# Kernel tuning notes

Hardware: AMD Instinct MI355X
Metric: run time of the kernel (lower is better)

## Reference

```python
import jax, jax.numpy as jnp
import numpy as np

N = 25600            # 64 graphs x 400 ROIs
F_IN = 400
H = 128
E = 512000           # 8000 edges per graph
B = 64
G = 8
OUT = 2
NPG = 400            # nodes per graph
EPG = E // B         # edges per graph
BN_EPS = 1e-5


def _xavier(k, shape):
    lim = float(np.sqrt(6.0 / (shape[0] + shape[1])))
    return jax.random.uniform(k, shape, jnp.float32, -lim, lim)


def setup_inputs() -> dict:
    key = jax.random.key(0)
    ks = jax.random.split(key, 16)
    inp = {}
    inp["x"] = jax.random.normal(ks[0], (N, F_IN), jnp.float32)
    # within-graph random edges: local index + graph offset
    src_l = jax.random.randint(ks[1], (E,), 0, NPG, jnp.int32)
    dst_l = jax.random.randint(ks[2], (E,), 0, NPG, jnp.int32)
    off = (jnp.arange(E, dtype=jnp.int32) // EPG) * NPG
    inp["edge_index"] = jnp.stack([src_l + off, dst_l + off])
    inp["batch"] = (jnp.arange(N, dtype=jnp.int32) // NPG)
    inp["group_ids"] = jax.random.randint(ks[3], (N,), 0, G, jnp.int32)
    inp["ge"] = _xavier(ks[4], (G, 2))
    inp["he"] = _xavier(ks[5], (2, 2))
    dims = [(F_IN + 4, H), (H, H), (H, H)]
    for i, (di, do) in enumerate(dims):
        k1, k2 = jax.random.split(ks[6 + i])
        inp[f"w{i}a"] = _xavier(k1, (di, do))
        inp[f"b{i}a"] = jnp.zeros((do,), jnp.float32)
        inp[f"g{i}"] = jnp.ones((do,), jnp.float32)
        inp[f"be{i}"] = jnp.zeros((do,), jnp.float32)
        inp[f"w{i}b"] = _xavier(k2, (do, do))
        inp[f"b{i}b"] = jnp.zeros((do,), jnp.float32)
    inp["wfa"] = _xavier(ks[10], (H, H))
    inp["bfa"] = jnp.zeros((H,), jnp.float32)
    inp["wfb"] = _xavier(ks[11], (H, OUT))
    inp["bfb"] = jnp.zeros((OUT,), jnp.float32)
    return inp


def _bn(h, gamma, beta):
    # BatchNorm1d in training mode: stats over node dimension
    mu = jnp.mean(h, axis=0, keepdims=True)
    var = jnp.var(h, axis=0, keepdims=True)
    return gamma * (h - mu) * jax.lax.rsqrt(var + BN_EPS) + beta


def reference(x, edge_index, batch, group_ids, ge, he,
              w0a, b0a, g0, be0, w0b, b0b,
              w1a, b1a, g1, be1, w1b, b1b,
              w2a, b2a, g2, be2, w2b, b2b,
              wfa, bfa, wfb, bfb):
    n = x.shape[0]
    hemi = jnp.arange(n) % 2                      # [1::2] = 1
    h = jnp.concatenate([x, ge[group_ids], he[hemi]], axis=-1)  # [N, F_IN+4]
    src, dst = edge_index[0], edge_index[1]
    layers = [(w0a, b0a, g0, be0, w0b, b0b),
              (w1a, b1a, g1, be1, w1b, b1b),
              (w2a, b2a, g2, be2, w2b, b2b)]
    for wa, ba, g, be, wb, bb in layers:
        # GINConv (eps=0): x_i + sum_{(j,i)} x_j, then 2-layer MLP w/ batchnorm
        agg = jax.ops.segment_sum(h[src], dst, num_segments=N)
        z = h + agg
        z = jax.nn.relu(_bn(z @ wa + ba, g, be))  # dropout = identity (eval)
        h = jax.nn.relu(z @ wb + bb)              # outer ReLU from forward()
    pooled = jax.ops.segment_sum(h, batch, num_segments=B)  # global_add_pool
    return jax.nn.relu(pooled @ wfa + bfa) @ wfb + bfb
```

## Files before the change

### kernel.cpp

```cpp
#include <hip/hip_runtime.h>

#define N_NODES 25600
#define F_IN 400
#define NE 512000
#define NB 64
#define NPG 400
#define EPG 8000
#define BN_EPS 1e-5f

#define S_ROWS 448
#define S_COLS 448
#define S_COLS2 (S_COLS / 2)
#define AGG_TILES 7
#define SB_RPB 112
#define K0PAD 448

typedef __attribute__((ext_vector_type(8))) short short8;
typedef __attribute__((ext_vector_type(4))) short short4_t;
typedef __attribute__((ext_vector_type(4))) float floatx4;

__device__ __forceinline__ unsigned short f2bf(float f) {
    unsigned int u = __float_as_uint(f);
    u += 0x7FFF + ((u >> 16) & 1);
    return (unsigned short)(u >> 16);
}
__device__ __forceinline__ float bf2f(unsigned short s) {
    return __uint_as_float((unsigned int)s << 16);
}
__device__ __forceinline__ short u8bf(unsigned v) {
    return (short)(__float_as_uint((float)v) >> 16);
}


__global__ __launch_bounds__(256) void prep(const int* __restrict__ src,
                                            const int* __restrict__ dst,
                                            unsigned char* __restrict__ Sb,
                                            const float* __restrict__ wa0, const float* __restrict__ wa1,
                                            const float* __restrict__ wa2, const float* __restrict__ wb0,
                                            const float* __restrict__ wb1, const float* __restrict__ wb2,
                                            unsigned short* __restrict__ t0, unsigned short* __restrict__ t1,
                                            unsigned short* __restrict__ t2, unsigned short* __restrict__ t3,
                                            unsigned short* __restrict__ t4, unsigned short* __restrict__ t5,
                                            float* __restrict__ pstat) {
    __shared__ int cnt32[SB_RPB * NPG / 4];
    int tid = threadIdx.x;
    if (blockIdx.x < 256) {
        int b = blockIdx.x;
        int g = b >> 2, part = b & 3;
        int r0 = part * SB_RPB;
        for (int i = tid; i < SB_RPB * NPG / 4; i += 256) cnt32[i] = 0;
        __syncthreads();
        int ebase = g * EPG, nbase = g * NPG;
        for (int e = tid; e < EPG; e += 256) {
            int d = dst[ebase + e] - nbase;
            int dr = d - r0;
            if ((unsigned)dr < (unsigned)SB_RPB) {
                int s = src[ebase + e] - nbase;
                int idx = dr * NPG + s;
                atomicAdd(&cnt32[idx >> 2], (int)(1u << ((idx & 3) * 8)));
            }
        }
        __syncthreads();
        const unsigned char* cb = (const unsigned char*)cnt32;
        for (int i = tid; i < SB_RPB * (S_COLS / 8); i += 256) {
            int rr = i / (S_COLS / 8), c8 = (i % (S_COLS / 8)) * 8;
            int R = r0 + rr;
            unsigned pk = 0;
#pragma unroll
            for (int j = 0; j < 8; ++j) {
                int c = c8 + j;
                unsigned v = 0;
                if (R < NPG && c < NPG) v = (unsigned)cb[rr * NPG + c] + (c == R ? 1u : 0u);
                pk |= (v & 15u) << (4 * j);
            }
            *(unsigned*)&Sb[((size_t)g * S_ROWS + R) * S_COLS2 + (c8 >> 1)] = pk;
        }
        return;
    }
    int idx = (blockIdx.x - 256) * 256 + tid;
    if (idx < 3 * 2048 + 8192) pstat[idx] = 0.f;
    if (idx < 128 * K0PAD) {
        int n = idx / K0PAD, k = idx - n * K0PAD;
        t0[idx] = (k < 400) ? f2bf(wa0[(size_t)k * 128 + n]) : (unsigned short)0;
        return;
    }
    idx -= 128 * K0PAD;
    if (idx >= 5 * 128 * 128) return;
    int seg = idx >> 14;
    int r = idx & 16383;
    int n = r >> 7, k = r & 127;
    const float* srcs[5] = {wb0, wa1, wb1, wa2, wb2};
    unsigned short* dsts[5] = {t3, t1, t4, t2, t5};
    dsts[seg][r] = f2bf(srcs[seg][(size_t)k * 128 + n]);
}


__global__ __launch_bounds__(256) void gemm_embed64(const float* __restrict__ A,
                                                    const unsigned short* __restrict__ Wt,
                                                    const float* __restrict__ Wfull,
                                                    const int* __restrict__ gid,
                                                    const float* __restrict__ ge,
                                                    const float* __restrict__ he,
                                                    unsigned short* __restrict__ CtT) {
    __shared__ __align__(16) unsigned short As[64][72];
    __shared__ __align__(16) unsigned short Bs[128][72];
    __shared__ float Wex[4][128];
    int tid = threadIdx.x;
    int m0 = blockIdx.x * 64;
    int wave = tid >> 6, lane = tid & 63;
    int wcol = wave * 32;
    int fm = lane & 15, quad = lane >> 4;

    for (int i = tid; i < 512; i += 256)
        Wex[i >> 7][i & 127] = Wfull[(size_t)(400 + (i >> 7)) * 128 + (i & 127)];

    floatx4 acc[4][2];
#pragma unroll
    for (int rt = 0; rt < 4; ++rt)
#pragma unroll
        for (int ct = 0; ct < 2; ++ct) acc[rt][ct] = (floatx4){0.f, 0.f, 0.f, 0.f};

    const int rA = tid >> 2, kcA = (tid & 3) * 16;
    const int nB = tid >> 1, kcB = (tid & 1) * 32;
    float4 aP0, aP1, aP2, aP3;
    short8 bP0, bP1, bP2, bP3;

    auto loadK = [&](int ks) {
        int k0 = ks * 64;
        int kg = k0 + kcA;
        const float* ar = A + (size_t)(m0 + rA) * F_IN;
        if (kg + 15 < 400) {
            aP0 = *(const float4*)(ar + kg);
            aP1 = *(const float4*)(ar + kg + 4);
            aP2 = *(const float4*)(ar + kg + 8);
            aP3 = *(const float4*)(ar + kg + 12);
        } else {
            float v[16];
#pragma unroll
            for (int j = 0; j < 16; ++j) v[j] = (kg + j < 400) ? ar[kg + j] : 0.f;
            aP0 = (float4){v[0], v[1], v[2], v[3]};
            aP1 = (float4){v[4], v[5], v[6], v[7]};
            aP2 = (float4){v[8], v[9], v[10], v[11]};
            aP3 = (float4){v[12], v[13], v[14], v[15]};
        }
        const unsigned short* wr = Wt + (size_t)nB * K0PAD + k0 + kcB;
        bP0 = *(const short8*)wr;
        bP1 = *(const short8*)(wr + 8);
        bP2 = *(const short8*)(wr + 16);
        bP3 = *(const short8*)(wr + 24);
    };

    loadK(0);
    for (int ks = 0; ks < 7; ++ks) {
        {
            short8 s0, s1;
            s0[0] = (short)f2bf(aP0.x); s0[1] = (short)f2bf(aP0.y);
            s0[2] = (short)f2bf(aP0.z); s0[3] = (short)f2bf(aP0.w);
            s0[4] = (short)f2bf(aP1.x); s0[5] = (short)f2bf(aP1.y);
            s0[6] = (short)f2bf(aP1.z); s0[7] = (short)f2bf(aP1.w);
            s1[0] = (short)f2bf(aP2.x); s1[1] = (short)f2bf(aP2.y);
            s1[2] = (short)f2bf(aP2.z); s1[3] = (short)f2bf(aP2.w);
            s1[4] = (short)f2bf(aP3.x); s1[5] = (short)f2bf(aP3.y);
            s1[6] = (short)f2bf(aP3.z); s1[7] = (short)f2bf(aP3.w);
            *(short8*)&As[rA][kcA] = s0;
            *(short8*)&As[rA][kcA + 8] = s1;
            *(short8*)&Bs[nB][kcB] = bP0;
            *(short8*)&Bs[nB][kcB + 8] = bP1;
            *(short8*)&Bs[nB][kcB + 16] = bP2;
            *(short8*)&Bs[nB][kcB + 24] = bP3;
        }
        __syncthreads();
        if (ks + 1 < 7) loadK(ks + 1);
#pragma unroll
        for (int k0l = 0; k0l < 64; k0l += 32) {
            short8 af[4], bf[2];
#pragma unroll
            for (int rt = 0; rt < 4; ++rt)
                af[rt] = *(const short8*)&As[rt * 16 + fm][k0l + quad * 8];
#pragma unroll
            for (int ct = 0; ct < 2; ++ct)
                bf[ct] = *(const short8*)&Bs[wcol + ct * 16 + fm][k0l + quad * 8];
#pragma unroll
            for (int rt = 0; rt < 4; ++rt)
#pragma unroll
                for (int ct = 0; ct < 2; ++ct)
                    acc[rt][ct] = __builtin_amdgcn_mfma_f32_16x16x32_bf16(
                        af[rt], bf[ct], acc[rt][ct], 0, 0, 0);
        }
        __syncthreads();
    }

#pragma unroll
    for (int rt = 0; rt < 4; ++rt) {
#pragma unroll
        for (int ct = 0; ct < 2; ++ct) {
            int col = wcol + ct * 16 + fm;
            int row0 = m0 + rt * 16 + quad * 4;
            ushort4 o;
#pragma unroll
            for (int r = 0; r < 4; ++r) {
                int row = row0 + r;
                int gv = gid[row];
                float v = acc[rt][ct][r]
                        + ge[gv * 2] * Wex[0][col] + ge[gv * 2 + 1] * Wex[1][col]
                        + he[(row & 1) * 2] * Wex[2][col] + he[(row & 1) * 2 + 1] * Wex[3][col];
                ((unsigned short*)&o)[r] = f2bf(v);
            }
            *(ushort4*)&CtT[(size_t)col * N_NODES + row0] = o;
        }
    }
}


__global__ __launch_bounds__(256) void agg_mfma(const unsigned char* __restrict__ Sb,
                                                const unsigned short* __restrict__ tT,
                                                const float* __restrict__ bias,
                                                unsigned short* __restrict__ z,
                                                float* __restrict__ psumG,
                                                float* __restrict__ psqG) {
    __shared__ __align__(16) unsigned short As[64][72];
    __shared__ __align__(16) unsigned short Bs[128][72];
    __shared__ float sw[4][2][16], qw[4][2][16];
    int tid = threadIdx.x;
    int b = blockIdx.x;
    int g = b & 63;
    int tile = b >> 6;
    int m0l = tile * 64;
    int node0 = g * NPG;
    int wave = tid >> 6, lane = tid & 63;
    int wcol = wave * 32;
    int fm = lane & 15, quad = lane >> 4;

    floatx4 acc[4][2];
#pragma unroll
    for (int rt = 0; rt < 4; ++rt)
#pragma unroll
        for (int ct = 0; ct < 2; ++ct) acc[rt][ct] = (floatx4){0.f, 0.f, 0.f, 0.f};

    const int rA = tid >> 2, kcA = (tid & 3) * 16;
    const int nB = tid >> 1, kcB = (tid & 1) * 32;
    unsigned long long aP;
    short8 bP0, bP1, bP2, bP3;

    auto loadK = [&](int ks) {
        int k0 = ks * 64;
        aP = *(const unsigned long long*)(Sb + ((size_t)g * S_ROWS + m0l + rA) * S_COLS2 + ((k0 + kcA) >> 1));
        const unsigned short* p = tT + (size_t)nB * N_NODES + node0 + k0 + kcB;
        bP0 = *(const short8*)p;
        bP1 = *(const short8*)(p + 8);
        bP2 = *(const short8*)(p + 16);
        bP3 = *(const short8*)(p + 24);
    };

    loadK(0);
    for (int ks = 0; ks < S_COLS / 64; ++ks) {
        {
            short8 s0, s1;
#pragma unroll
            for (int j = 0; j < 8; ++j) s0[j] = u8bf((unsigned)(aP >> (4 * j)) & 15u);
#pragma unroll
            for (int j = 0; j < 8; ++j) s1[j] = u8bf((unsigned)(aP >> (32 + 4 * j)) & 15u);
            *(short8*)&As[rA][kcA] = s0;
            *(short8*)&As[rA][kcA + 8] = s1;
            *(short8*)&Bs[nB][kcB] = bP0;
            *(short8*)&Bs[nB][kcB + 8] = bP1;
            *(short8*)&Bs[nB][kcB + 16] = bP2;
            *(short8*)&Bs[nB][kcB + 24] = bP3;
        }
        __syncthreads();
        if (ks + 1 < S_COLS / 64) loadK(ks + 1);
#pragma unroll
        for (int k0l = 0; k0l < 64; k0l += 32) {
            short8 af[4], bf[2];
#pragma unroll
            for (int rt = 0; rt < 4; ++rt)
                af[rt] = *(const short8*)&As[rt * 16 + fm][k0l + quad * 8];
#pragma unroll
            for (int ct = 0; ct < 2; ++ct)
                bf[ct] = *(const short8*)&Bs[wcol + ct * 16 + fm][k0l + quad * 8];
#pragma unroll
            for (int rt = 0; rt < 4; ++rt)
#pragma unroll
                for (int ct = 0; ct < 2; ++ct)
                    acc[rt][ct] = __builtin_amdgcn_mfma_f32_16x16x32_bf16(
                        af[rt], bf[ct], acc[rt][ct], 0, 0, 0);
        }
        __syncthreads();
    }

    {
        float scol[2] = {0.f, 0.f}, qcol[2] = {0.f, 0.f};
#pragma unroll
        for (int rt = 0; rt < 4; ++rt) {
#pragma unroll
            for (int ct = 0; ct < 2; ++ct) {
                int col = wcol + ct * 16 + fm;
                float bv = bias[col];
                int rbase = m0l + rt * 16 + quad * 4;
#pragma unroll
                for (int r = 0; r < 4; ++r) {
                    int rloc = rbase + r;
                    if (rloc < NPG) {
                        float v = acc[rt][ct][r] + bv;
                        z[(size_t)(node0 + rloc) * 128 + col] = f2bf(v);
                        scol[ct] += v;
                        qcol[ct] += v * v;
                    }
                }
            }
        }
#pragma unroll
        for (int ct = 0; ct < 2; ++ct) {
            scol[ct] += __shfl_xor(scol[ct], 16);
            scol[ct] += __shfl_xor(scol[ct], 32);
            qcol[ct] += __shfl_xor(qcol[ct], 16);
            qcol[ct] += __shfl_xor(qcol[ct], 32);
        }
        if (lane < 16) {
#pragma unroll
            for (int ct = 0; ct < 2; ++ct) { sw[wave][ct][lane] = scol[ct]; qw[wave][ct][lane] = qcol[ct]; }
        }
    }
    __syncthreads();
    if (tid < 128) {
        int c = tid;
        int wv = c >> 5, ct = (c >> 4) & 1, f = c & 15;
        int bucket = b & 7;
        atomicAdd(&psumG[bucket * 128 + c], sw[wv][ct][f]);
        atomicAdd(&psqG[bucket * 128 + c], qw[wv][ct][f]);
    }
}


#define MODE_FUSED 0
#define MODE_FINAL 1

template <int MODE>
__global__ __launch_bounds__(256) void gemm_post64(const unsigned short* __restrict__ z,
                                                   const float* __restrict__ psumG,
                                                   const float* __restrict__ psqG,
                                                   const float* __restrict__ gamma,
                                                   const float* __restrict__ beta,
                                                   const unsigned short* __restrict__ wtb,
                                                   const float* __restrict__ bb,
                                                   const unsigned short* __restrict__ wta_next,
                                                   unsigned short* __restrict__ CtT,
                                                   float* __restrict__ pooled) {
    __shared__ __align__(16) unsigned short Bs[128][72];
    __shared__ __align__(16) unsigned short hs[64][136];
    __shared__ float coefs[256];
    int tid = threadIdx.x;
    int m0 = blockIdx.x * 64;
    int wave = tid >> 6, lane = tid & 63;
    int wcol = wave * 32;
    int fm = lane & 15, quad = lane >> 4;

    if (tid < 128) {
        float S = 0.f, Q = 0.f;
#pragma unroll
        for (int b = 0; b < 8; ++b) { S += psumG[b * 128 + tid]; Q += psqG[b * 128 + tid]; }
        float invn = 1.0f / (float)N_NODES;
        float mu = S * invn;
        float var = Q * invn - mu * mu;
        float a = gamma[tid] * rsqrtf(var + BN_EPS);
        coefs[tid] = a;
        coefs[128 + tid] = beta[tid] - a * mu;
    }
    __syncthreads();

    floatx4 acc[4][2];
#pragma unroll
    for (int rt = 0; rt < 4; ++rt)
#pragma unroll
        for (int ct = 0; ct < 2; ++ct) acc[rt][ct] = (floatx4){0.f, 0.f, 0.f, 0.f};

    const int rA = tid >> 2, kcA = (tid & 3) * 16;
    const int nB = tid >> 1, kcB = (tid & 1) * 32;
    short8 aPa, aPb;
    short8 bP0, bP1, bP2, bP3;

    auto loadK1 = [&](int ks) {
        int k0 = ks * 64;
        const unsigned short* zr = &z[(size_t)(m0 + rA) * 128 + k0 + kcA];
        aPa = *(const short8*)zr;
        aPb = *(const short8*)(zr + 8);
        const unsigned short* wr = wtb + (size_t)nB * 128 + k0 + kcB;
        bP0 = *(const short8*)wr;
        bP1 = *(const short8*)(wr + 8);
        bP2 = *(const short8*)(wr + 16);
        bP3 = *(const short8*)(wr + 24);
    };

    loadK1(0);
    for (int ks = 0; ks < 2; ++ks) {
        {
            int kg = ks * 64 + kcA;
            short8 s0, s1;
#pragma unroll
            for (int j = 0; j < 8; ++j) {
                float v = fmaxf(coefs[kg + j] * bf2f((unsigned short)aPa[j]) + coefs[128 + kg + j], 0.f);
                s0[j] = (short)f2bf(v);
            }
#pragma unroll
            for (int j = 0; j < 8; ++j) {
                float v = fmaxf(coefs[kg + 8 + j] * bf2f((unsigned short)aPb[j]) + coefs[128 + kg + 8 + j], 0.f);
                s1[j] = (short)f2bf(v);
            }
            *(short8*)&hs[rA][kcA] = s0;
            *(short8*)&hs[rA][kcA + 8] = s1;
            *(short8*)&Bs[nB][kcB] = bP0;
            *(short8*)&Bs[nB][kcB + 8] = bP1;
            *(short8*)&Bs[nB][kcB + 16] = bP2;
            *(short8*)&Bs[nB][kcB + 24] = bP3;
        }
        __syncthreads();
        if (ks + 1 < 2) loadK1(ks + 1);
#pragma unroll
        for (int k0l = 0; k0l < 64; k0l += 32) {
            short8 af[4], bf[2];
#pragma unroll
            for (int rt = 0; rt < 4; ++rt)
                af[rt] = *(const short8*)&hs[rt * 16 + fm][k0l + quad * 8];
#pragma unroll
            for (int ct = 0; ct < 2; ++ct)
                bf[ct] = *(const short8*)&Bs[wcol + ct * 16 + fm][k0l + quad * 8];
#pragma unroll
            for (int rt = 0; rt < 4; ++rt)
#pragma unroll
                for (int ct = 0; ct < 2; ++ct)
                    acc[rt][ct] = __builtin_amdgcn_mfma_f32_16x16x32_bf16(
                        af[rt], bf[ct], acc[rt][ct], 0, 0, 0);
        }
        __syncthreads();
    }

    if (MODE == MODE_FINAL) {
        float rsum[4][2];
#pragma unroll
        for (int rt = 0; rt < 4; ++rt)
#pragma unroll
            for (int ct = 0; ct < 2; ++ct) {
                int col = wcol + ct * 16 + fm;
                float bv = bb[col];
                float s = 0.f;
#pragma unroll
                for (int r = 0; r < 4; ++r) s += fmaxf(acc[rt][ct][r] + bv, 0.f);
                rsum[rt][ct] = s;
            }
        bool uniform = (m0 / NPG) == ((m0 + 63) / NPG);
        if (uniform) {
            int gph = m0 / NPG;
#pragma unroll
            for (int ct = 0; ct < 2; ++ct) {
                float cs = rsum[0][ct] + rsum[1][ct] + rsum[2][ct] + rsum[3][ct];
                cs += __shfl_xor(cs, 16);
                cs += __shfl_xor(cs, 32);
                if (lane < 16) atomicAdd(&pooled[gph * 128 + wcol + ct * 16 + fm], cs);
            }
        } else {
#pragma unroll
            for (int rt = 0; rt < 4; ++rt)
#pragma unroll
                for (int ct = 0; ct < 2; ++ct) {
                    int gph = (m0 + rt * 16 + quad * 4) / NPG;
                    atomicAdd(&pooled[gph * 128 + wcol + ct * 16 + fm], rsum[rt][ct]);
                }
        }
        return;
    }

#pragma unroll
    for (int rt = 0; rt < 4; ++rt)
#pragma unroll
        for (int ct = 0; ct < 2; ++ct) {
            int col = wcol + ct * 16 + fm;
            float bv = bb[col];
            int rbase = rt * 16 + quad * 4;
#pragma unroll
            for (int r = 0; r < 4; ++r)
                hs[rbase + r][col] = f2bf(fmaxf(acc[rt][ct][r] + bv, 0.f));
        }
    __syncthreads();

#pragma unroll
    for (int rt = 0; rt < 4; ++rt)
#pragma unroll
        for (int ct = 0; ct < 2; ++ct) acc[rt][ct] = (floatx4){0.f, 0.f, 0.f, 0.f};

    const int kcB2 = (tid & 1) * 16;
    for (int ks = 0; ks < 4; ++ks) {
        int k0 = ks * 32;
        {
            const unsigned short* wr = wta_next + (size_t)nB * 128 + k0 + kcB2;
            *(short8*)&Bs[nB][kcB2] = *(const short8*)wr;
            *(short8*)&Bs[nB][kcB2 + 8] = *(const short8*)(wr + 8);
        }
        __syncthreads();
        {
            short8 af[4], bf[2];
#pragma unroll
            for (int rt = 0; rt < 4; ++rt)
                af[rt] = *(const short8*)&hs[rt * 16 + fm][k0 + quad * 8];
#pragma unroll
            for (int ct = 0; ct < 2; ++ct)
                bf[ct] = *(const short8*)&Bs[wcol + ct * 16 + fm][quad * 8];
#pragma unroll
            for (int rt = 0; rt < 4; ++rt)
#pragma unroll
                for (int ct = 0; ct < 2; ++ct)
                    acc[rt][ct] = __builtin_amdgcn_mfma_f32_16x16x32_bf16(
                        af[rt], bf[ct], acc[rt][ct], 0, 0, 0);
        }
        __syncthreads();
    }

#pragma unroll
    for (int rt = 0; rt < 4; ++rt)
#pragma unroll
        for (int ct = 0; ct < 2; ++ct) {
            int col = wcol + ct * 16 + fm;
            int row0 = m0 + rt * 16 + quad * 4;
            ushort4 o;
#pragma unroll
            for (int r = 0; r < 4; ++r) ((unsigned short*)&o)[r] = f2bf(acc[rt][ct][r]);
            *(ushort4*)&CtT[(size_t)col * N_NODES + row0] = o;
        }
}


__global__ __launch_bounds__(128) void head(const float* __restrict__ pooled,
                                            const float* __restrict__ wfa,
                                            const float* __restrict__ bfa,
                                            const float* __restrict__ wfb,
                                            const float* __restrict__ bfb,
                                            float* __restrict__ out) {
    int g = blockIdx.x;
    int f = threadIdx.x;
    __shared__ float pl[128];
    pl[f] = pooled[g * 128 + f];
    __syncthreads();
    float a = bfa[f];
    for (int k = 0; k < 128; ++k) a += pl[k] * wfa[k * 128 + f];
    float p2 = fmaxf(a, 0.f);
    __shared__ float o0[128], o1[128];
    o0[f] = p2 * wfb[f * 2 + 0];
    o1[f] = p2 * wfb[f * 2 + 1];
    __syncthreads();
    if (f == 0) {
        float a0 = bfb[0], a1 = bfb[1];
#pragma unroll
        for (int k = 0; k < 128; ++k) { a0 += o0[k]; a1 += o1[k]; }
        out[g * 2 + 0] = a0;
        out[g * 2 + 1] = a1;
    }
}


extern "C" void kernel_launch(void* const* d_in, const int* in_sizes, int n_in,
                              void* d_out, int out_size, void* d_ws, size_t ws_size,
                              hipStream_t stream) {
    const float* x   = (const float*)d_in[0];
    const int* ei    = (const int*)d_in[1];
    const int* gid   = (const int*)d_in[3];
    const float* ge  = (const float*)d_in[4];
    const float* he  = (const float*)d_in[5];
    const float* wa[3] = {(const float*)d_in[6],  (const float*)d_in[12], (const float*)d_in[18]};
    const float* ba[3] = {(const float*)d_in[7],  (const float*)d_in[13], (const float*)d_in[19]};
    const float* gg[3] = {(const float*)d_in[8],  (const float*)d_in[14], (const float*)d_in[20]};
    const float* bb_[3]= {(const float*)d_in[9],  (const float*)d_in[15], (const float*)d_in[21]};
    const float* wb[3] = {(const float*)d_in[10], (const float*)d_in[16], (const float*)d_in[22]};
    const float* bbias[3] = {(const float*)d_in[11], (const float*)d_in[17], (const float*)d_in[23]};
    const float* wfa = (const float*)d_in[24];
    const float* bfa = (const float*)d_in[25];
    const float* wfb = (const float*)d_in[26];
    const float* bfb = (const float*)d_in[27];
    float* out = (float*)d_out;

    char* ws = (char*)d_ws;
    size_t o = 0;
    auto alloc = [&](size_t bytes) { char* p = ws + o; o += (bytes + 255) & ~(size_t)255; return p; };
    unsigned short* tT = (unsigned short*)alloc((size_t)128 * N_NODES * 2 + 1024);
    unsigned short* z  = (unsigned short*)alloc((size_t)N_NODES * 128 * 2);
    unsigned char* Sb  = (unsigned char*)alloc((size_t)NB * S_ROWS * S_COLS2);
    float* pstat = (float*)alloc((3 * 2048 + 8192) * 4);
    unsigned short* wt0  = (unsigned short*)alloc(128 * K0PAD * 2);
    unsigned short* wta1 = (unsigned short*)alloc(128 * 128 * 2);
    unsigned short* wta2 = (unsigned short*)alloc(128 * 128 * 2);
    unsigned short* wtb0 = (unsigned short*)alloc(128 * 128 * 2);
    unsigned short* wtb1 = (unsigned short*)alloc(128 * 128 * 2);
    unsigned short* wtb2 = (unsigned short*)alloc(128 * 128 * 2);
    (void)ws_size; (void)in_sizes; (void)n_in; (void)out_size;

    const int* esrc_in = ei;
    const int* edst_in = ei + NE;

    prep<<<256 + 544, 256, 0, stream>>>(esrc_in, edst_in, Sb,
                                        wa[0], wa[1], wa[2], wb[0], wb[1], wb[2],
                                        wt0, wta1, wta2, wtb0, wtb1, wtb2, pstat);

    float* ps0 = pstat;            float* pq0 = pstat + 1024;
    float* ps1 = pstat + 2048;     float* pq1 = pstat + 3072;
    float* ps2 = pstat + 4096;     float* pq2 = pstat + 5120;
    float* pooled = pstat + 6144;

    gemm_embed64<<<400, 256, 0, stream>>>(x, wt0, wa[0], gid, ge, he, tT);
    agg_mfma<<<NB * AGG_TILES, 256, 0, stream>>>(Sb, tT, ba[0], z, ps0, pq0);
    gemm_post64<MODE_FUSED><<<400, 256, 0, stream>>>(z, ps0, pq0, gg[0], bb_[0],
                                                     wtb0, bbias[0], wta1, tT, nullptr);
    agg_mfma<<<NB * AGG_TILES, 256, 0, stream>>>(Sb, tT, ba[1], z, ps1, pq1);
    gemm_post64<MODE_FUSED><<<400, 256, 0, stream>>>(z, ps1, pq1, gg[1], bb_[1],
                                                     wtb1, bbias[1], wta2, tT, nullptr);
    agg_mfma<<<NB * AGG_TILES, 256, 0, stream>>>(Sb, tT, ba[2], z, ps2, pq2);
    gemm_post64<MODE_FINAL><<<400, 256, 0, stream>>>(z, ps2, pq2, gg[2], bb_[2],
                                                     wtb2, bbias[2], nullptr, nullptr, pooled);

    head<<<NB, 128, 0, stream>>>(pooled, wfa, bfa, wfb, bfb, out);
}
```

Before: 254.1 us.

## Fuse all GIN stages into one persistent kernel with grid-wide barriers

Replaces the nine separate launches (prep, embed, three agg/post pairs, head) with one persistent kernel of 448 blocks that runs each phase in turn, separated by a software grid barrier built on atomics. Shared memory is carved by hand per phase, and the weight-transpose prep loops over several passes so fewer blocks cover it. This removes launch overhead and inter-kernel gaps. In exchange it relies on all 448 blocks being co-resident (launch_bounds 256,2) and adds barrier spin cost plus a memset per call.

```diff
diff --git a/kernel.cpp b/kernel.cpp
--- a/kernel.cpp
+++ b/kernel.cpp
@@ -11,13 +11,26 @@
 #define S_ROWS 448
 #define S_COLS 448
 #define S_COLS2 (S_COLS / 2)
-#define AGG_TILES 7
 #define SB_RPB 112
 #define K0PAD 448
 
+#define NBLK 448
+
+#define TT_OFF    0u
+#define Z_OFF     6555648u
+#define SB_OFF    13109248u
+#define PSTAT_OFF 19531776u
+#define WT0_OFF   19589120u
+#define WTA1_OFF  19703808u
+#define WTA2_OFF  19736576u
+#define WTB0_OFF  19769344u
+#define WTB1_OFF  19802112u
+#define WTB2_OFF  19834880u
+#define BAR_OFF   19867648u
+
 typedef __attribute__((ext_vector_type(8))) short short8;
-typedef __attribute__((ext_vector_type(4))) short short4_t;
 typedef __attribute__((ext_vector_type(4))) float floatx4;
+typedef unsigned short us;
 
 __device__ __forceinline__ unsigned short f2bf(float f) {
     unsigned int u = __float_as_uint(f);
@@ -31,22 +44,33 @@
     return (short)(__float_as_uint((float)v) >> 16);
 }
 
-
-__global__ __launch_bounds__(256) void prep(const int* __restrict__ src,
-                                            const int* __restrict__ dst,
-                                            unsigned char* __restrict__ Sb,
-                                            const float* __restrict__ wa0, const float* __restrict__ wa1,
-                                            const float* __restrict__ wa2, const float* __restrict__ wb0,
-                                            const float* __restrict__ wb1, const float* __restrict__ wb2,
-                                            unsigned short* __restrict__ t0, unsigned short* __restrict__ t1,
-                                            unsigned short* __restrict__ t2, unsigned short* __restrict__ t3,
-                                            unsigned short* __restrict__ t4, unsigned short* __restrict__ t5,
-                                            float* __restrict__ pstat) {
-    __shared__ int cnt32[SB_RPB * NPG / 4];
-    int tid = threadIdx.x;
-    if (blockIdx.x < 256) {
-        int b = blockIdx.x;
-        int g = b >> 2, part = b & 3;
+__device__ __forceinline__ void gsync(unsigned* bar) {
+    __syncthreads();
+    if (threadIdx.x == 0) {
+        unsigned gen = __hip_atomic_load(bar + 16, __ATOMIC_ACQUIRE, __HIP_MEMORY_SCOPE_AGENT);
+        __threadfence();
+        if (__hip_atomic_fetch_add(bar, 1u, __ATOMIC_ACQ_REL, __HIP_MEMORY_SCOPE_AGENT) == NBLK - 1u) {
+            __hip_atomic_store(bar, 0u, __ATOMIC_RELAXED, __HIP_MEMORY_SCOPE_AGENT);
+            __hip_atomic_fetch_add(bar + 16, 1u, __ATOMIC_RELEASE, __HIP_MEMORY_SCOPE_AGENT);
+        } else {
+            while (__hip_atomic_load(bar + 16, __ATOMIC_RELAXED, __HIP_MEMORY_SCOPE_AGENT) == gen)
+                __builtin_amdgcn_s_sleep(8);
+        }
+        __threadfence();
+    }
+    __syncthreads();
+}
+
+
+__device__ __forceinline__ void phase_prep(unsigned char* smem, int bid, int tid,
+        const int* __restrict__ src, const int* __restrict__ dst, unsigned char* Sb,
+        const float* __restrict__ wa0, const float* __restrict__ wa1, const float* __restrict__ wa2,
+        const float* __restrict__ wb0, const float* __restrict__ wb1, const float* __restrict__ wb2,
+        us* wt0, us* wta1, us* wta2, us* wtb0, us* wtb1, us* wtb2,
+        float* pstat, us* tT) {
+    if (bid < 256) {
+        int* cnt32 = (int*)smem;
+        int g = bid >> 2, part = bid & 3;
         int r0 = part * SB_RPB;
         for (int i = tid; i < SB_RPB * NPG / 4; i += 256) cnt32[i] = 0;
         __syncthreads();
@@ -75,38 +99,38 @@
             }
             *(unsigned*)&Sb[((size_t)g * S_ROWS + R) * S_COLS2 + (c8 >> 1)] = pk;
         }
-        return;
-    }
-    int idx = (blockIdx.x - 256) * 256 + tid;
-    if (idx < 3 * 2048 + 8192) pstat[idx] = 0.f;
-    if (idx < 128 * K0PAD) {
-        int n = idx / K0PAD, k = idx - n * K0PAD;
-        t0[idx] = (k < 400) ? f2bf(wa0[(size_t)k * 128 + n]) : (unsigned short)0;
-        return;
-    }
-    idx -= 128 * K0PAD;
-    if (idx >= 5 * 128 * 128) return;
-    int seg = idx >> 14;
-    int r = idx & 16383;
-    int n = r >> 7, k = r & 127;
-    const float* srcs[5] = {wb0, wa1, wb1, wa2, wb2};
-    unsigned short* dsts[5] = {t3, t1, t4, t2, t5};
-    dsts[seg][r] = f2bf(srcs[seg][(size_t)k * 128 + n]);
-}
-
-
-__global__ __launch_bounds__(256) void gemm_embed64(const float* __restrict__ A,
-                                                    const unsigned short* __restrict__ Wt,
-                                                    const float* __restrict__ Wfull,
-                                                    const int* __restrict__ gid,
-                                                    const float* __restrict__ ge,
-                                                    const float* __restrict__ he,
-                                                    unsigned short* __restrict__ CtT) {
-    __shared__ __align__(16) unsigned short As[64][72];
-    __shared__ __align__(16) unsigned short Bs[128][72];
-    __shared__ float Wex[4][128];
-    int tid = threadIdx.x;
-    int m0 = blockIdx.x * 64;
+    } else {
+        int base0 = (bid - 256) * 256 + tid;
+        if (base0 < 3 * 2048 + 8192) pstat[base0] = 0.f;
+        if (base0 < 512) tT[(size_t)128 * N_NODES + base0] = 0;
+#pragma unroll 1
+        for (int pass = 0; pass < 3; ++pass) {
+            int idx = base0 + pass * 49152;
+            if (idx < 128 * K0PAD) {
+                int n = idx / K0PAD, k = idx - n * K0PAD;
+                wt0[idx] = (k < 400) ? f2bf(wa0[(size_t)k * 128 + n]) : (unsigned short)0;
+            } else if (idx < 128 * K0PAD + 5 * 16384) {
+                int r2 = idx - 128 * K0PAD;
+                int seg = r2 >> 14, r = r2 & 16383;
+                int n = r >> 7, k = r & 127;
+                const float* s5[5] = {wb0, wa1, wb1, wa2, wb2};
+                us* d5[5] = {wtb0, wta1, wtb1, wta2, wtb2};
+                d5[seg][r] = f2bf(s5[seg][(size_t)k * 128 + n]);
+            }
+        }
+    }
+}
+
+
+__device__ __forceinline__ void phase_embed(unsigned char* smem, int bid, int tid,
+        const float* __restrict__ A, const us* Wt, const float* __restrict__ Wfull,
+        const int* __restrict__ gid, const float* __restrict__ ge, const float* __restrict__ he,
+        us* CtT) {
+    if (bid >= 400) return;
+    us (*As)[72] = (us(*)[72])smem;
+    us (*Bs)[72] = (us(*)[72])(smem + 9216);
+    float (*Wex)[128] = (float(*)[128])(smem + 27648);
+    int m0 = bid * 64;
     int wave = tid >> 6, lane = tid & 63;
     int wcol = wave * 32;
     int fm = lane & 15, quad = lane >> 4;
@@ -143,7 +167,7 @@
             aP2 = (float4){v[8], v[9], v[10], v[11]};
             aP3 = (float4){v[12], v[13], v[14], v[15]};
         }
-        const unsigned short* wr = Wt + (size_t)nB * K0PAD + k0 + kcB;
+        const us* wr = Wt + (size_t)nB * K0PAD + k0 + kcB;
         bP0 = *(const short8*)wr;
         bP1 = *(const short8*)(wr + 8);
         bP2 = *(const short8*)(wr + 16);
@@ -212,19 +236,15 @@
 }
 
 
-__global__ __launch_bounds__(256) void agg_mfma(const unsigned char* __restrict__ Sb,
-                                                const unsigned short* __restrict__ tT,
-                                                const float* __restrict__ bias,
-                                                unsigned short* __restrict__ z,
-                                                float* __restrict__ psumG,
-                                                float* __restrict__ psqG) {
-    __shared__ __align__(16) unsigned short As[64][72];
-    __shared__ __align__(16) unsigned short Bs[128][72];
-    __shared__ float sw[4][2][16], qw[4][2][16];
-    int tid = threadIdx.x;
-    int b = blockIdx.x;
-    int g = b & 63;
-    int tile = b >> 6;
+__device__ __forceinline__ void phase_agg(unsigned char* smem, int bid, int tid,
+        const unsigned char* Sb, const us* tT, const float* __restrict__ bias,
+        us* z, float* psumG, float* psqG) {
+    us (*As)[72] = (us(*)[72])smem;
+    us (*Bs)[72] = (us(*)[72])(smem + 9216);
+    float (*sw)[2][16] = (float(*)[2][16])(smem + 27648);
+    float (*qw)[2][16] = (float(*)[2][16])(smem + 28160);
+    int g = bid & 63;
+    int tile = bid >> 6;
     int m0l = tile * 64;
     int node0 = g * NPG;
     int wave = tid >> 6, lane = tid & 63;
@@ -245,7 +265,7 @@
     auto loadK = [&](int ks) {
         int k0 = ks * 64;
         aP = *(const unsigned long long*)(Sb + ((size_t)g * S_ROWS + m0l + rA) * S_COLS2 + ((k0 + kcA) >> 1));
-        const unsigned short* p = tT + (size_t)nB * N_NODES + node0 + k0 + kcB;
+        const us* p = tT + (size_t)nB * N_NODES + node0 + k0 + kcB;
         bP0 = *(const short8*)p;
         bP1 = *(const short8*)(p + 8);
         bP2 = *(const short8*)(p + 16);
@@ -325,7 +345,7 @@
     if (tid < 128) {
         int c = tid;
         int wv = c >> 5, ct = (c >> 4) & 1, f = c & 15;
-        int bucket = b & 7;
+        int bucket = bid & 7;
         atomicAdd(&psumG[bucket * 128 + c], sw[wv][ct][f]);
         atomicAdd(&psqG[bucket * 128 + c], qw[wv][ct][f]);
     }
@@ -336,21 +356,16 @@
 #define MODE_FINAL 1
 
 template <int MODE>
-__global__ __launch_bounds__(256) void gemm_post64(const unsigned short* __restrict__ z,
-                                                   const float* __restrict__ psumG,
-                                                   const float* __restrict__ psqG,
-                                                   const float* __restrict__ gamma,
-                                                   const float* __restrict__ beta,
-                                                   const unsigned short* __restrict__ wtb,
-                                                   const float* __restrict__ bb,
-                                                   const unsigned short* __restrict__ wta_next,
-                                                   unsigned short* __restrict__ CtT,
-                                                   float* __restrict__ pooled) {
-    __shared__ __align__(16) unsigned short Bs[128][72];
-    __shared__ __align__(16) unsigned short hs[64][136];
-    __shared__ float coefs[256];
-    int tid = threadIdx.x;
-    int m0 = blockIdx.x * 64;
+__device__ __forceinline__ void phase_post(unsigned char* smem, int bid, int tid,
+        const us* z, const float* psumG, const float* psqG,
+        const float* __restrict__ gamma, const float* __restrict__ beta,
+        const us* wtb, const float* __restrict__ bb,
+        const us* wta_next, us* CtT, float* pooled) {
+    if (bid >= 400) return;
+    us (*hs)[136] = (us(*)[136])smem;
+    us (*Bs)[72]  = (us(*)[72])(smem + 17408);
+    float* coefs  = (float*)(smem + 35840);
+    int m0 = bid * 64;
     int wave = tid >> 6, lane = tid & 63;
     int wcol = wave * 32;
     int fm = lane & 15, quad = lane >> 4;
@@ -381,10 +396,10 @@
 
     auto loadK1 = [&](int ks) {
         int k0 = ks * 64;
-        const unsigned short* zr = &z[(size_t)(m0 + rA) * 128 + k0 + kcA];
+        const us* zr = &z[(size_t)(m0 + rA) * 128 + k0 + kcA];
         aPa = *(const short8*)zr;
         aPb = *(const short8*)(zr + 8);
-        const unsigned short* wr = wtb + (size_t)nB * 128 + k0 + kcB;
+        const us* wr = wtb + (size_t)nB * 128 + k0 + kcB;
         bP0 = *(const short8*)wr;
         bP1 = *(const short8*)(wr + 8);
         bP2 = *(const short8*)(wr + 16);
@@ -491,7 +506,7 @@
     for (int ks = 0; ks < 4; ++ks) {
         int k0 = ks * 32;
         {
-            const unsigned short* wr = wta_next + (size_t)nB * 128 + k0 + kcB2;
+            const us* wr = wta_next + (size_t)nB * 128 + k0 + kcB2;
             *(short8*)&Bs[nB][kcB2] = *(const short8*)wr;
             *(short8*)&Bs[nB][kcB2 + 8] = *(const short8*)(wr + 8);
         }
@@ -528,30 +543,76 @@
 }
 
 
-__global__ __launch_bounds__(128) void head(const float* __restrict__ pooled,
-                                            const float* __restrict__ wfa,
-                                            const float* __restrict__ bfa,
-                                            const float* __restrict__ wfb,
-                                            const float* __restrict__ bfb,
-                                            float* __restrict__ out) {
-    int g = blockIdx.x;
-    int f = threadIdx.x;
-    __shared__ float pl[128];
-    pl[f] = pooled[g * 128 + f];
-    __syncthreads();
-    float a = bfa[f];
-    for (int k = 0; k < 128; ++k) a += pl[k] * wfa[k * 128 + f];
-    float p2 = fmaxf(a, 0.f);
-    __shared__ float o0[128], o1[128];
-    o0[f] = p2 * wfb[f * 2 + 0];
-    o1[f] = p2 * wfb[f * 2 + 1];
-    __syncthreads();
-    if (f == 0) {
-        float a0 = bfb[0], a1 = bfb[1];
-#pragma unroll
-        for (int k = 0; k < 128; ++k) { a0 += o0[k]; a1 += o1[k]; }
-        out[g * 2 + 0] = a0;
-        out[g * 2 + 1] = a1;
+__global__ __launch_bounds__(256, 2) void fused_all(
+        const float* __restrict__ x, const int* __restrict__ esrc, const int* __restrict__ edst,
+        const int* __restrict__ gid, const float* __restrict__ ge, const float* __restrict__ he,
+        const float* __restrict__ wa0, const float* __restrict__ ba0, const float* __restrict__ gg0,
+        const float* __restrict__ be0, const float* __restrict__ wb0, const float* __restrict__ bbias0,
+        const float* __restrict__ wa1, const float* __restrict__ ba1, const float* __restrict__ gg1,
+        const float* __restrict__ be1, const float* __restrict__ wb1, const float* __restrict__ bbias1,
+        const float* __restrict__ wa2, const float* __restrict__ ba2, const float* __restrict__ gg2,
+        const float* __restrict__ be2, const float* __restrict__ wb2, const float* __restrict__ bbias2,
+        const float* __restrict__ wfa, const float* __restrict__ bfa,
+        const float* __restrict__ wfb, const float* __restrict__ bfb,
+        float* __restrict__ out, unsigned char* ws) {
+    __shared__ __align__(16) unsigned char smem[44800];
+    us* tT = (us*)(ws + TT_OFF);
+    us* z  = (us*)(ws + Z_OFF);
+    unsigned char* Sb = ws + SB_OFF;
+    float* pstat = (float*)(ws + PSTAT_OFF);
+    us* wt0  = (us*)(ws + WT0_OFF);
+    us* wta1 = (us*)(ws + WTA1_OFF);
+    us* wta2 = (us*)(ws + WTA2_OFF);
+    us* wtb0 = (us*)(ws + WTB0_OFF);
+    us* wtb1 = (us*)(ws + WTB1_OFF);
+    us* wtb2 = (us*)(ws + WTB2_OFF);
+    unsigned* bar = (unsigned*)(ws + BAR_OFF);
+    float* pooled = pstat + 6144;
+    int bid = blockIdx.x, tid = threadIdx.x;
+
+    phase_prep(smem, bid, tid, esrc, edst, Sb, wa0, wa1, wa2, wb0, wb1, wb2,
+               wt0, wta1, wta2, wtb0, wtb1, wtb2, pstat, tT);
+    gsync(bar);
+    phase_embed(smem, bid, tid, x, wt0, wa0, gid, ge, he, tT);
+    gsync(bar);
+    phase_agg(smem, bid, tid, Sb, tT, ba0, z, pstat + 0, pstat + 1024);
+    gsync(bar);
+    phase_post<MODE_FUSED>(smem, bid, tid, z, pstat + 0, pstat + 1024, gg0, be0,
+                           wtb0, bbias0, wta1, tT, nullptr);
+    gsync(bar);
+    phase_agg(smem, bid, tid, Sb, tT, ba1, z, pstat + 2048, pstat + 3072);
+    gsync(bar);
+    phase_post<MODE_FUSED>(smem, bid, tid, z, pstat + 2048, pstat + 3072, gg1, be1,
+                           wtb1, bbias1, wta2, tT, nullptr);
+    gsync(bar);
+    phase_agg(smem, bid, tid, Sb, tT, ba2, z, pstat + 4096, pstat + 5120);
+    gsync(bar);
+    phase_post<MODE_FINAL>(smem, bid, tid, z, pstat + 4096, pstat + 5120, gg2, be2,
+                           wtb2, bbias2, nullptr, nullptr, pooled);
+    gsync(bar);
+
+    if (bid < 64) {
+        float* pl = (float*)smem;
+        float* o0 = (float*)smem + 128;
+        float* o1 = (float*)smem + 256;
+        int f = tid;
+        if (f < 128) pl[f] = pooled[bid * 128 + f];
+        __syncthreads();
+        if (f < 128) {
+            float a = bfa[f];
+            for (int k = 0; k < 128; ++k) a += pl[k] * wfa[k * 128 + f];
+            float p2 = fmaxf(a, 0.f);
+            o0[f] = p2 * wfb[f * 2 + 0];
+            o1[f] = p2 * wfb[f * 2 + 1];
+        }
+        __syncthreads();
+        if (f == 0) {
+            float a0 = bfb[0], a1 = bfb[1];
+#pragma unroll
+            for (int k = 0; k < 128; ++k) { a0 += o0[k]; a1 += o1[k]; }
+            out[bid * 2 + 0] = a0;
+            out[bid * 2 + 1] = a1;
+        }
     }
 }
 
@@ -564,55 +625,21 @@
     const int* gid   = (const int*)d_in[3];
     const float* ge  = (const float*)d_in[4];
     const float* he  = (const float*)d_in[5];
-    const float* wa[3] = {(const float*)d_in[6],  (const float*)d_in[12], (const float*)d_in[18]};
-    const float* ba[3] = {(const float*)d_in[7],  (const float*)d_in[13], (const float*)d_in[19]};
-    const float* gg[3] = {(const float*)d_in[8],  (const float*)d_in[14], (const float*)d_in[20]};
-    const float* bb_[3]= {(const float*)d_in[9],  (const float*)d_in[15], (const float*)d_in[21]};
-    const float* wb[3] = {(const float*)d_in[10], (const float*)d_in[16], (const float*)d_in[22]};
-    const float* bbias[3] = {(const float*)d_in[11], (const float*)d_in[17], (const float*)d_in[23]};
-    const float* wfa = (const float*)d_in[24];
-    const float* bfa = (const float*)d_in[25];
-    const float* wfb = (const float*)d_in[26];
-    const float* bfb = (const float*)d_in[27];
     float* out = (float*)d_out;
-
-    char* ws = (char*)d_ws;
-    size_t o = 0;
-    auto alloc = [&](size_t bytes) { char* p = ws + o; o += (bytes + 255) & ~(size_t)255; return p; };
-    unsigned short* tT = (unsigned short*)alloc((size_t)128 * N_NODES * 2 + 1024);
-    unsigned short* z  = (unsigned short*)alloc((size_t)N_NODES * 128 * 2);
-    unsigned char* Sb  = (unsigned char*)alloc((size_t)NB * S_ROWS * S_COLS2);
-    float* pstat = (float*)alloc((3 * 2048 + 8192) * 4);
-    unsigned short* wt0  = (unsigned short*)alloc(128 * K0PAD * 2);
-    unsigned short* wta1 = (unsigned short*)alloc(128 * 128 * 2);
-    unsigned short* wta2 = (unsigned short*)alloc(128 * 128 * 2);
-    unsigned short* wtb0 = (unsigned short*)alloc(128 * 128 * 2);
-    unsigned short* wtb1 = (unsigned short*)alloc(128 * 128 * 2);
-    unsigned short* wtb2 = (unsigned short*)alloc(128 * 128 * 2);
+    unsigned char* ws = (unsigned char*)d_ws;
     (void)ws_size; (void)in_sizes; (void)n_in; (void)out_size;
 
-    const int* esrc_in = ei;
-    const int* edst_in = ei + NE;
-
-    prep<<<256 + 544, 256, 0, stream>>>(esrc_in, edst_in, Sb,
-                                        wa[0], wa[1], wa[2], wb[0], wb[1], wb[2],
-                                        wt0, wta1, wta2, wtb0, wtb1, wtb2, pstat);
-
-    float* ps0 = pstat;            float* pq0 = pstat + 1024;
-    float* ps1 = pstat + 2048;     float* pq1 = pstat + 3072;
-    float* ps2 = pstat + 4096;     float* pq2 = pstat + 5120;
-    float* pooled = pstat + 6144;
-
-    gemm_embed64<<<400, 256, 0, stream>>>(x, wt0, wa[0], gid, ge, he, tT);
-    agg_mfma<<<NB * AGG_TILES, 256, 0, stream>>>(Sb, tT, ba[0], z, ps0, pq0);
-    gemm_post64<MODE_FUSED><<<400, 256, 0, stream>>>(z, ps0, pq0, gg[0], bb_[0],
-                                                     wtb0, bbias[0], wta1, tT, nullptr);
-    agg_mfma<<<NB * AGG_TILES, 256, 0, stream>>>(Sb, tT, ba[1], z, ps1, pq1);
-    gemm_post64<MODE_FUSED><<<400, 256, 0, stream>>>(z, ps1, pq1, gg[1], bb_[1],
-                                                     wtb1, bbias[1], wta2, tT, nullptr);
-    agg_mfma<<<NB * AGG_TILES, 256, 0, stream>>>(Sb, tT, ba[2], z, ps2, pq2);
-    gemm_post64<MODE_FINAL><<<400, 256, 0, stream>>>(z, ps2, pq2, gg[2], bb_[2],
-                                                     wtb2, bbias[2], nullptr, nullptr, pooled);
-
-    head<<<NB, 128, 0, stream>>>(pooled, wfa, bfa, wfb, bfb, out);
-}
+    hipMemsetAsync(ws + BAR_OFF, 0, 256, stream);
+
+    fused_all<<<NBLK, 256, 0, stream>>>(
+        x, ei, ei + NE, gid, ge, he,
+        (const float*)d_in[6],  (const float*)d_in[7],  (const float*)d_in[8],
+        (const float*)d_in[9],  (const float*)d_in[10], (const float*)d_in[11],
+        (const float*)d_in[12], (const float*)d_in[13], (const float*)d_in[14],
+        (const float*)d_in[15], (const float*)d_in[16], (const float*)d_in[17],
+        (const float*)d_in[18], (const float*)d_in[19], (const float*)d_in[20],
+        (const float*)d_in[21], (const float*)d_in[22], (const float*)d_in[23],
+        (const float*)d_in[24], (const float*)d_in[25],
+        (const float*)d_in[26], (const float*)d_in[27],
+        out, ws);
+}
```

Result: slower. 739.8 us (+191.2%).
